# Performance work log

Hardware: AMD Instinct MI355X
Metric: run time of the kernel (lower is better)

Reference implementation:

```python
import jax, jax.numpy as jnp
import numpy as np

N_NODES = 100000
FEAT = 64
HID = 128
N_EDGES = 1200000


def setup_inputs() -> dict:
    key = jax.random.key(0)
    ks = jax.random.split(key, 8)
    x = jax.random.normal(ks[0], (N_NODES, FEAT), dtype=jnp.float32)
    edge_index = jax.random.randint(ks[1], (2, N_EDGES), 0, N_NODES, dtype=jnp.int32)
    # SAGEConv params: lin_l (on aggregated neighbors, with bias), lin_r (on root, no bias)
    W1l = jax.random.normal(ks[2], (HID, FEAT), jnp.float32) / np.float32(np.sqrt(FEAT))
    b1l = jnp.zeros((HID,), jnp.float32)
    W1r = jax.random.normal(ks[3], (HID, FEAT), jnp.float32) / np.float32(np.sqrt(FEAT))
    W2l = jax.random.normal(ks[4], (FEAT, HID), jnp.float32) / np.float32(np.sqrt(HID))
    b2l = jnp.zeros((FEAT,), jnp.float32)
    W2r = jax.random.normal(ks[5], (FEAT, HID), jnp.float32) / np.float32(np.sqrt(HID))
    return {"x": x, "edge_index": edge_index, "W1l": W1l, "b1l": b1l,
            "W1r": W1r, "W2l": W2l, "b2l": b2l, "W2r": W2r}


def _sage_conv(x, src, dst, Wl, bl, Wr, n_nodes):
    # mean aggregation of neighbor messages x[src] at targets dst
    msg = x[src]                                                  # [E, d]
    agg = jax.ops.segment_sum(msg, dst, num_segments=n_nodes)     # [N, d]
    deg = jax.ops.segment_sum(jnp.ones((src.shape[0],), x.dtype), dst,
                              num_segments=n_nodes)               # [N]
    agg = agg / jnp.maximum(deg, 1.0)[:, None]
    # out = lin_l(agg) + lin_r(x); lin_r has no bias (PyG SAGEConv default)
    return agg @ Wl.T + bl + x @ Wr.T


def reference(x, edge_index, W1l, b1l, W1r, W2l, b2l, W2r):
    src, dst = edge_index[0], edge_index[1]
    n = x.shape[0]
    h = jax.nn.relu(_sage_conv(x, src, dst, W1l, b1l, W1r, n))
    # dropout(p=0.5) is identity in eval mode
    out = _sage_conv(h, src, dst, W2l, b2l, W2r, n)
    return out
```

## Files before the change

### kernel.cpp

```cpp
#include <hip/hip_runtime.h>
#include <hip/hip_bf16.h>

typedef __bf16 bf16;
typedef __attribute__((ext_vector_type(8))) __bf16 bf16x8;
typedef __attribute__((ext_vector_type(4))) float f32x4;

#define NBLK 256

__device__ inline void unpack8(uint4 r, f32x4& a, f32x4& b) {
  a.x = __uint_as_float(r.x << 16);
  a.y = __uint_as_float(r.x & 0xffff0000u);
  a.z = __uint_as_float(r.y << 16);
  a.w = __uint_as_float(r.y & 0xffff0000u);
  b.x = __uint_as_float(r.z << 16);
  b.y = __uint_as_float(r.z & 0xffff0000u);
  b.z = __uint_as_float(r.w << 16);
  b.w = __uint_as_float(r.w & 0xffff0000u);
}

__device__ inline uint4 slot_load(const bf16* __restrict__ tab, const int* __restrict__ nbr,
                                  int base, int e, int q, int fo) {
  int idx = base + q;
  uint4 r = make_uint4(0u, 0u, 0u, 0u);
  if (idx < e) {
    int j = nbr[idx];
    r = *(const uint4*)(tab + j * 64 + fo);
  }
  return r;
}

__global__ __launch_bounds__(256) void setup_k(const float* __restrict__ x,
                                               const int* __restrict__ dst,
                                               const float* __restrict__ W1l,
                                               const float* __restrict__ W1r,
                                               const float* __restrict__ W2l,
                                               const float* __restrict__ W2r,
                                               bf16* __restrict__ xb,
                                               bf16* __restrict__ B1,
                                               bf16* __restrict__ B2,
                                               int* __restrict__ hist,
                                               int E, int nb, int N, int Np) {
  __shared__ int h[1024];
  int t = threadIdx.x;
  if (blockIdx.x < NBLK) {
    for (int i = t; i < nb; i += 256) h[i] = 0;
    __syncthreads();
    int chunk = (E + NBLK - 1) / NBLK;
    int s = blockIdx.x * chunk, e = min(E, s + chunk);
    for (int i = s + t; i < e; i += 256) atomicAdd(&h[dst[i] >> 7], 1);
    __syncthreads();
    for (int i = t; i < nb; i += 256) hist[(long)i * NBLK + blockIdx.x] = h[i];
  } else if (blockIdx.x < NBLK + 128) {
    int gid = (blockIdx.x - NBLK) * 256 + t;
    if (gid < 16384) {
      int c = gid >> 7, k = gid & 127;
      float v = (k < 64) ? W1l[c * 64 + k] : W1r[c * 64 + (k - 64)];
      B1[gid] = (bf16)v;
    } else {
      int idx = gid - 16384;
      int n = idx >> 7, k = idx & 127;
      float v = (n < 64) ? W2l[n * 128 + k] : W2r[(n - 64) * 128 + k];
      B2[idx] = (bf16)v;
    }
  } else {
    int gid = (blockIdx.x - NBLK - 128) * 256 + t;
    long base = (long)gid * 4;
    if (base >= (long)Np * 64) return;
    if (base < (long)N * 64) {
      f32x4 v = *(const f32x4*)(x + base);
      bf16 o[4] = {(bf16)v.x, (bf16)v.y, (bf16)v.z, (bf16)v.w};
      *(ulong1*)(xb + base) = *(ulong1*)o;
    } else {
      bf16 o[4] = {(bf16)0.0f, (bf16)0.0f, (bf16)0.0f, (bf16)0.0f};
      *(ulong1*)(xb + base) = *(ulong1*)o;
    }
  }
}

__global__ __launch_bounds__(256) void scanA_k(int* __restrict__ hist,
                                               int* __restrict__ bsum) {
  __shared__ int sd[256];
  int t = threadIdx.x;
  int idx = blockIdx.x * 256 + t;
  int v = hist[idx];
  sd[t] = v;
  __syncthreads();
#pragma unroll
  for (int off = 1; off < 256; off <<= 1) {
    int tv = (t >= off) ? sd[t - off] : 0;
    __syncthreads();
    if (t >= off) sd[t] += tv;
    __syncthreads();
  }
  hist[idx] = sd[t] - v;
  if (t == 255) bsum[blockIdx.x] = sd[255];
}

__global__ __launch_bounds__(1024) void scanB_k(int* __restrict__ bsum, int nb) {
  __shared__ int sd[1024];
  int t = threadIdx.x;
  int v = (t < nb) ? bsum[t] : 0;
  sd[t] = v;
  __syncthreads();
#pragma unroll
  for (int off = 1; off < 1024; off <<= 1) {
    int tv = (t >= off) ? sd[t - off] : 0;
    __syncthreads();
    if (t >= off) sd[t] += tv;
    __syncthreads();
  }
  if (t < nb) bsum[t] = sd[t] - v;
}

__global__ __launch_bounds__(512) void scat_k(const int* __restrict__ src,
                                              const int* __restrict__ dst,
                                              const int* __restrict__ hist,
                                              const int* __restrict__ bsum,
                                              unsigned* __restrict__ ebuf, int E, int nb) {
  __shared__ int cur[1024];
  for (int i = threadIdx.x; i < nb; i += 512)
    cur[i] = bsum[i] + hist[(long)i * NBLK + blockIdx.x];
  __syncthreads();
  int chunk = (E + NBLK - 1) / NBLK;
  int s = blockIdx.x * chunk, e = min(E, s + chunk);
  for (int i = s + threadIdx.x; i < e; i += 512) {
    int d = dst[i];
    int pos = atomicAdd(&cur[d >> 7], 1);
    ebuf[pos] = ((unsigned)src[i] << 7) | (unsigned)(d & 127);
  }
}

__global__ __launch_bounds__(256) void csr_k(const unsigned* __restrict__ ebuf,
                                             const int* __restrict__ bsum,
                                             int* __restrict__ rowptr,
                                             int* __restrict__ nbr, int nb, int Np, int E) {
  __shared__ int hcnt[128];
  __shared__ int hoff[128];
  int b = blockIdx.x, t = threadIdx.x;
  int s = bsum[b];
  int e = (b + 1 < nb) ? bsum[b + 1] : E;
  if (t < 128) hcnt[t] = 0;
  __syncthreads();
  for (int i = s + t; i < e; i += 256) atomicAdd(&hcnt[ebuf[i] & 127u], 1);
  __syncthreads();
  if (t < 128) hoff[t] = hcnt[t];
  __syncthreads();
#pragma unroll
  for (int off = 1; off < 128; off <<= 1) {
    int v = (t < 128 && t >= off) ? hoff[t - off] : 0;
    __syncthreads();
    if (t < 128 && t >= off) hoff[t] += v;
    __syncthreads();
  }
  if (t < 128) {
    int ex = hoff[t] - hcnt[t];
    rowptr[b * 128 + t] = s + ex;
    hcnt[t] = ex;
  }
  if (blockIdx.x == gridDim.x - 1 && t == 0) rowptr[Np] = E;
  __syncthreads();
  for (int i = s + t; i < e; i += 256) {
    unsigned r = ebuf[i];
    int pos = atomicAdd(&hcnt[r & 127u], 1);
    nbr[s + pos] = (int)(r >> 7);
  }
}

__global__ __launch_bounds__(256) void agg1_k(const bf16* __restrict__ xb,
                                              const int* __restrict__ rowptr,
                                              const int* __restrict__ nbr,
                                              bf16* __restrict__ A1, int Np) {
  int wave = threadIdx.x >> 6, lane = threadIdx.x & 63;
  int n0 = (blockIdx.x * 4 + wave) * 4;
  if (n0 >= Np) return;
  int q = lane >> 3, f = lane & 7;
  int fo = f * 8;
  int s[4], e[4];
#pragma unroll
  for (int m = 0; m < 4; m++) { s[m] = rowptr[n0 + m]; e[m] = rowptr[n0 + m + 1]; }
  uint4 c0[4], c1[4];
#pragma unroll
  for (int m = 0; m < 2; m++) {
    c0[m] = slot_load(xb, nbr, s[m], e[m], q, fo);
    c1[m] = slot_load(xb, nbr, s[m] + 8, e[m], q, fo);
  }
  uint4 rvc = (q == 1) ? *(const uint4*)(xb + (long)n0 * 64 + fo)
                       : make_uint4(0u, 0u, 0u, 0u);
#pragma unroll
  for (int m = 0; m < 4; m++) {
    if (m + 2 < 4) {
      c0[m + 2] = slot_load(xb, nbr, s[m + 2], e[m + 2], q, fo);
      c1[m + 2] = slot_load(xb, nbr, s[m + 2] + 8, e[m + 2], q, fo);
    }
    uint4 rvn = (q == 1 && m + 1 < 4)
                    ? *(const uint4*)(xb + (long)(n0 + m + 1) * 64 + fo)
                    : make_uint4(0u, 0u, 0u, 0u);
    f32x4 sa = {0, 0, 0, 0}, sb = {0, 0, 0, 0};
    uint4 a0 = c0[m], a1 = c1[m];
    if (s[m] + 16 < e[m]) {
      for (int i = s[m] + 16; i < e[m]; i += 16) {
        uint4 t0 = slot_load(xb, nbr, i, e[m], q, fo);
        uint4 t1 = slot_load(xb, nbr, i + 8, e[m], q, fo);
        f32x4 a, b;
        unpack8(a0, a, b); sa += a; sb += b;
        unpack8(a1, a, b); sa += a; sb += b;
        a0 = t0; a1 = t1;
      }
    }
    {
      f32x4 a, b;
      unpack8(a0, a, b); sa += a; sb += b;
      unpack8(a1, a, b); sa += a; sb += b;
    }
    float v[8] = {sa.x, sa.y, sa.z, sa.w, sb.x, sb.y, sb.z, sb.w};
#pragma unroll
    for (int k = 0; k < 8; k++) {
      v[k] += __shfl_xor(v[k], 8);
      v[k] += __shfl_xor(v[k], 16);
      v[k] += __shfl_xor(v[k], 32);
    }
    float invd = 1.0f / fmaxf((float)(e[m] - s[m]), 1.0f);
    if (q == 0) {
      bf16x8 o = {(bf16)(v[0] * invd), (bf16)(v[1] * invd), (bf16)(v[2] * invd),
                  (bf16)(v[3] * invd), (bf16)(v[4] * invd), (bf16)(v[5] * invd),
                  (bf16)(v[6] * invd), (bf16)(v[7] * invd)};
      *(bf16x8*)(A1 + (long)(n0 + m) * 128 + fo) = o;
    } else if (q == 1) {
      *(uint4*)(A1 + (long)(n0 + m) * 128 + 64 + fo) = rvc;
    }
    rvc = rvn;
  }
}

__device__ inline int swzoff(int r, int x) {
  return r * 256 + (x ^ (((r & 3) << 6) ^ ((r & 7) << 4)));
}

__global__ __launch_bounds__(256) void fused_k(const bf16* __restrict__ A,
                                               const bf16* __restrict__ B1g,
                                               const bf16* __restrict__ B2g,
                                               const float* __restrict__ b1l,
                                               bf16* __restrict__ Ct,
                                               bf16* __restrict__ Cu, int T) {
  __shared__ __align__(16) char Asm[2][8192];
  __shared__ __align__(16) char Hsm[8192];
  int tid = threadIdx.x;
  int wave = tid >> 6, lane = tid & 63;
  int row = lane & 15, quad = lane >> 4;
  int cb = wave * 32;

  bf16x8 b1f[2][4], b2f[2][4];
#pragma unroll
  for (int jj = 0; jj < 2; jj++)
#pragma unroll
    for (int s = 0; s < 4; s++) {
      b1f[jj][s] = *(const bf16x8*)(B1g + (cb + jj * 16 + row) * 128 + s * 32 + quad * 8);
      b2f[jj][s] = *(const bf16x8*)(B2g + (cb + jj * 16 + row) * 128 + s * 32 + quad * 8);
    }
  float bias[2] = {b1l[cb + row], b1l[cb + 16 + row]};

  int srow = wave * 8 + quad;
  int schunk = row;

  int t = blockIdx.x;
  {
    uint4 v0 = *(const uint4*)(A + ((long)t * 32 + srow) * 128 + schunk * 8);
    uint4 v1 = *(const uint4*)(A + ((long)t * 32 + srow + 4) * 128 + schunk * 8);
    *(uint4*)(Asm[0] + swzoff(srow, schunk * 16)) = v0;
    *(uint4*)(Asm[0] + swzoff(srow + 4, schunk * 16)) = v1;
  }
  __syncthreads();

  int p = 0;
  for (; t < T; t += (int)gridDim.x, p ^= 1) {
    int tn = t + (int)gridDim.x;
    bool pf = tn < T;
    uint4 v0 = {}, v1 = {};
    if (pf) {
      v0 = *(const uint4*)(A + ((long)tn * 32 + srow) * 128 + schunk * 8);
      v1 = *(const uint4*)(A + ((long)tn * 32 + srow + 4) * 128 + schunk * 8);
    }
    f32x4 acc1[2][2] = {};
#pragma unroll
    for (int s = 0; s < 4; s++) {
#pragma unroll
      for (int st = 0; st < 2; st++) {
        bf16x8 a = *(const bf16x8*)(Asm[p] + swzoff(st * 16 + row, s * 64 + quad * 16));
#pragma unroll
        for (int jj = 0; jj < 2; jj++)
          acc1[st][jj] = __builtin_amdgcn_mfma_f32_16x16x32_bf16(a, b1f[jj][s], acc1[st][jj], 0, 0, 0);
      }
    }
#pragma unroll
    for (int st = 0; st < 2; st++)
#pragma unroll
      for (int jj = 0; jj < 2; jj++)
#pragma unroll
        for (int i = 0; i < 4; i++) {
          float v = acc1[st][jj][i] + bias[jj];
          v = v > 0.0f ? v : 0.0f;
          *(bf16*)(Hsm + swzoff(st * 16 + quad * 4 + i, (cb + jj * 16 + row) * 2)) = (bf16)v;
        }
    __syncthreads();
    f32x4 acc2[2][2] = {};
#pragma unroll
    for (int s = 0; s < 4; s++) {
#pragma unroll
      for (int st = 0; st < 2; st++) {
        bf16x8 a = *(const bf16x8*)(Hsm + swzoff(st * 16 + row, s * 64 + quad * 16));
#pragma unroll
        for (int jj = 0; jj < 2; jj++)
          acc2[st][jj] = __builtin_amdgcn_mfma_f32_16x16x32_bf16(a, b2f[jj][s], acc2[st][jj], 0, 0, 0);
      }
    }
    bf16* outp = (wave < 2) ? Ct : Cu;
    int oc = cb + row - ((wave < 2) ? 0 : 64);
#pragma unroll
    for (int st = 0; st < 2; st++)
#pragma unroll
      for (int jj = 0; jj < 2; jj++)
#pragma unroll
        for (int i = 0; i < 4; i++) {
          long grow = (long)t * 32 + st * 16 + quad * 4 + i;
          outp[grow * 64 + oc + jj * 16] = (bf16)acc2[st][jj][i];
        }
    if (pf) {
      *(uint4*)(Asm[p ^ 1] + swzoff(srow, schunk * 16)) = v0;
      *(uint4*)(Asm[p ^ 1] + swzoff(srow + 4, schunk * 16)) = v1;
    }
    __syncthreads();
  }
}

__global__ __launch_bounds__(256) void agg2_k(const bf16* __restrict__ tmat,
                                              const bf16* __restrict__ umat,
                                              const int* __restrict__ rowptr,
                                              const int* __restrict__ nbr,
                                              const float* __restrict__ b2l,
                                              float* __restrict__ out, int N) {
  int wave = threadIdx.x >> 6, lane = threadIdx.x & 63;
  int n = blockIdx.x * 4 + wave;
  if (n >= N) return;
  int s = rowptr[n], e = rowptr[n + 1];
  int q = lane >> 3, f = lane & 7;
  int fo = f * 8;
  f32x4 sa = {0, 0, 0, 0}, sb = {0, 0, 0, 0};
  uint4 c0 = slot_load(tmat, nbr, s, e, q, fo);
  uint4 c1 = slot_load(tmat, nbr, s + 8, e, q, fo);
  int i = s + 16;
  for (; i < e; i += 16) {
    uint4 n0 = slot_load(tmat, nbr, i, e, q, fo);
    uint4 n1 = slot_load(tmat, nbr, i + 8, e, q, fo);
    f32x4 a, b;
    unpack8(c0, a, b); sa += a; sb += b;
    unpack8(c1, a, b); sa += a; sb += b;
    c0 = n0; c1 = n1;
  }
  {
    f32x4 a, b;
    unpack8(c0, a, b); sa += a; sb += b;
    unpack8(c1, a, b); sa += a; sb += b;
  }
  float v[8] = {sa.x, sa.y, sa.z, sa.w, sb.x, sb.y, sb.z, sb.w};
#pragma unroll
  for (int k = 0; k < 8; k++) {
    v[k] += __shfl_xor(v[k], 8);
    v[k] += __shfl_xor(v[k], 16);
    v[k] += __shfl_xor(v[k], 32);
  }
  if (q == 0) {
    float invd = 1.0f / fmaxf((float)(e - s), 1.0f);
    f32x4 b0 = *(const f32x4*)(b2l + fo);
    f32x4 b1 = *(const f32x4*)(b2l + fo + 4);
    f32x4 ua, ub;
    unpack8(*(const uint4*)(umat + n * 64 + fo), ua, ub);
    f32x4 o0, o1;
    o0.x = v[0] * invd + b0.x + ua.x;
    o0.y = v[1] * invd + b0.y + ua.y;
    o0.z = v[2] * invd + b0.z + ua.z;
    o0.w = v[3] * invd + b0.w + ua.w;
    o1.x = v[4] * invd + b1.x + ub.x;
    o1.y = v[5] * invd + b1.y + ub.y;
    o1.z = v[6] * invd + b1.z + ub.z;
    o1.w = v[7] * invd + b1.w + ub.w;
    *(f32x4*)(out + n * 64 + fo) = o0;
    *(f32x4*)(out + n * 64 + fo + 4) = o1;
  }
}

static inline size_t align256(size_t x) { return (x + 255) / 256 * 256; }

extern "C" void kernel_launch(void* const* d_in, const int* in_sizes, int n_in,
                              void* d_out, int out_size, void* d_ws, size_t ws_size,
                              hipStream_t stream) {
  const float* x = (const float*)d_in[0];
  const int* edge_index = (const int*)d_in[1];
  const float* W1l = (const float*)d_in[2];
  const float* b1l = (const float*)d_in[3];
  const float* W1r = (const float*)d_in[4];
  const float* W2l = (const float*)d_in[5];
  const float* b2l = (const float*)d_in[6];
  const float* W2r = (const float*)d_in[7];

  const int N = in_sizes[0] / 64;
  const int E = in_sizes[1] / 2;
  const int Np = (N + 127) / 128 * 128;
  const int nb = Np / 128;
  const int M = nb * NBLK;

  const int* src = edge_index;
  const int* dst = edge_index + E;

  char* ws = (char*)d_ws;
  size_t off = 0;
  int* hist = (int*)(ws + off);           off += align256((size_t)M * 4);
  int* bsum = (int*)(ws + off);           off += align256((size_t)nb * 4);
  int* rowptr = (int*)(ws + off);         off += align256((size_t)(Np + 1) * 4);
  unsigned* ebuf = (unsigned*)(ws + off); off += align256((size_t)E * 4);
  int* nbr = (int*)(ws + off);            off += align256((size_t)E * 4);
  bf16* xb = (bf16*)(ws + off);           off += align256((size_t)Np * 64 * 2);
  bf16* A1 = (bf16*)(ws + off);           off += align256((size_t)Np * 128 * 2);
  bf16* tmat = (bf16*)(ws + off);         off += align256((size_t)Np * 64 * 2);
  bf16* umat = (bf16*)(ws + off);         off += align256((size_t)Np * 64 * 2);
  bf16* B1 = (bf16*)(ws + off);           off += align256(128 * 128 * 2);
  bf16* B2 = (bf16*)(ws + off);           off += align256(128 * 128 * 2);
  float* out = (float*)d_out;

  const int cvtBlocks = (int)(((long)Np * 64 / 4 + 255) / 256);
  setup_k<<<NBLK + 128 + cvtBlocks, 256, 0, stream>>>(x, dst, W1l, W1r, W2l, W2r,
                                                      xb, B1, B2, hist, E, nb, N, Np);
  scanA_k<<<nb, 256, 0, stream>>>(hist, bsum);
  scanB_k<<<1, 1024, 0, stream>>>(bsum, nb);
  scat_k<<<NBLK, 512, 0, stream>>>(src, dst, hist, bsum, ebuf, E, nb);
  csr_k<<<nb, 256, 0, stream>>>(ebuf, bsum, rowptr, nbr, nb, Np, E);

  agg1_k<<<Np / 16, 256, 0, stream>>>(xb, rowptr, nbr, A1, Np);
  fused_k<<<1564, 256, 0, stream>>>(A1, B1, B2, b1l, tmat, umat, Np / 32);
  agg2_k<<<(N + 3) / 4, 256, 0, stream>>>(tmat, umat, rowptr, nbr, b2l, out, N);
}
```

Measured before the change: 220.2 us.

## Build CSR with per-node global atomic counting and scatter instead of two-level bucket sort

```diff
diff --git a/kernel.cpp b/kernel.cpp
--- a/kernel.cpp
+++ b/kernel.cpp
@@ -4,8 +4,6 @@
 typedef __bf16 bf16;
 typedef __attribute__((ext_vector_type(8))) __bf16 bf16x8;
 typedef __attribute__((ext_vector_type(4))) float f32x4;
-
-#define NBLK 256
 
 __device__ inline void unpack8(uint4 r, f32x4& a, f32x4& b) {
   a.x = __uint_as_float(r.x << 16);
@@ -29,29 +27,21 @@
   return r;
 }
 
-__global__ __launch_bounds__(256) void setup_k(const float* __restrict__ x,
-                                               const int* __restrict__ dst,
-                                               const float* __restrict__ W1l,
-                                               const float* __restrict__ W1r,
-                                               const float* __restrict__ W2l,
-                                               const float* __restrict__ W2r,
-                                               bf16* __restrict__ xb,
-                                               bf16* __restrict__ B1,
-                                               bf16* __restrict__ B2,
-                                               int* __restrict__ hist,
-                                               int E, int nb, int N, int Np) {
-  __shared__ int h[1024];
+
+__global__ __launch_bounds__(256) void zero_k(const float* __restrict__ W1l,
+                                              const float* __restrict__ W1r,
+                                              const float* __restrict__ W2l,
+                                              const float* __restrict__ W2r,
+                                              bf16* __restrict__ B1,
+                                              bf16* __restrict__ B2,
+                                              int* __restrict__ deg,
+                                              int Np, int nscan) {
   int t = threadIdx.x;
-  if (blockIdx.x < NBLK) {
-    for (int i = t; i < nb; i += 256) h[i] = 0;
-    __syncthreads();
-    int chunk = (E + NBLK - 1) / NBLK;
-    int s = blockIdx.x * chunk, e = min(E, s + chunk);
-    for (int i = s + t; i < e; i += 256) atomicAdd(&h[dst[i] >> 7], 1);
-    __syncthreads();
-    for (int i = t; i < nb; i += 256) hist[(long)i * NBLK + blockIdx.x] = h[i];
-  } else if (blockIdx.x < NBLK + 128) {
-    int gid = (blockIdx.x - NBLK) * 256 + t;
+  if ((int)blockIdx.x < nscan) {
+    int idx = blockIdx.x * 256 + t;
+    if (idx < Np) deg[idx] = 0;
+  } else {
+    int gid = ((int)blockIdx.x - nscan) * 256 + t;
     if (gid < 16384) {
       int c = gid >> 7, k = gid & 127;
       float v = (k < 64) ? W1l[c * 64 + k] : W1r[c * 64 + (k - 64)];
@@ -62,8 +52,20 @@
       float v = (n < 64) ? W2l[n * 128 + k] : W2r[(n - 64) * 128 + k];
       B2[idx] = (bf16)v;
     }
+  }
+}
+
+__global__ __launch_bounds__(256) void setup_k(const float* __restrict__ x,
+                                               const int* __restrict__ dst,
+                                               int* __restrict__ deg,
+                                               bf16* __restrict__ xb,
+                                               int E, int N, int Np) {
+  int t = threadIdx.x;
+  if (blockIdx.x < 256) {
+    for (int i = blockIdx.x * 256 + t; i < E; i += 256 * 256)
+      atomicAdd(&deg[dst[i]], 1);
   } else {
-    int gid = (blockIdx.x - NBLK - 128) * 256 + t;
+    int gid = (blockIdx.x - 256) * 256 + t;
     long base = (long)gid * 4;
     if (base >= (long)Np * 64) return;
     if (base < (long)N * 64) {
@@ -77,12 +79,13 @@
   }
 }
 
-__global__ __launch_bounds__(256) void scanA_k(int* __restrict__ hist,
-                                               int* __restrict__ bsum) {
+__global__ __launch_bounds__(256) void scan256_k(const int* __restrict__ deg,
+                                                 int* __restrict__ tmp,
+                                                 int* __restrict__ bsum, int Np) {
   __shared__ int sd[256];
   int t = threadIdx.x;
   int idx = blockIdx.x * 256 + t;
-  int v = hist[idx];
+  int v = (idx < Np) ? deg[idx] : 0;
   sd[t] = v;
   __syncthreads();
 #pragma unroll
@@ -92,77 +95,48 @@
     if (t >= off) sd[t] += tv;
     __syncthreads();
   }
-  hist[idx] = sd[t] - v;
+  if (idx < Np) tmp[idx] = sd[t] - v;
   if (t == 255) bsum[blockIdx.x] = sd[255];
 }
 
-__global__ __launch_bounds__(1024) void scanB_k(int* __restrict__ bsum, int nb) {
-  __shared__ int sd[1024];
+__global__ __launch_bounds__(512) void scanS_k(int* __restrict__ bsum, int nv) {
+  __shared__ int sd[512];
   int t = threadIdx.x;
-  int v = (t < nb) ? bsum[t] : 0;
+  int v = (t < nv) ? bsum[t] : 0;
   sd[t] = v;
   __syncthreads();
 #pragma unroll
-  for (int off = 1; off < 1024; off <<= 1) {
+  for (int off = 1; off < 512; off <<= 1) {
     int tv = (t >= off) ? sd[t - off] : 0;
     __syncthreads();
     if (t >= off) sd[t] += tv;
     __syncthreads();
   }
-  if (t < nb) bsum[t] = sd[t] - v;
-}
-
-__global__ __launch_bounds__(512) void scat_k(const int* __restrict__ src,
-                                              const int* __restrict__ dst,
-                                              const int* __restrict__ hist,
-                                              const int* __restrict__ bsum,
-                                              unsigned* __restrict__ ebuf, int E, int nb) {
-  __shared__ int cur[1024];
-  for (int i = threadIdx.x; i < nb; i += 512)
-    cur[i] = bsum[i] + hist[(long)i * NBLK + blockIdx.x];
-  __syncthreads();
-  int chunk = (E + NBLK - 1) / NBLK;
-  int s = blockIdx.x * chunk, e = min(E, s + chunk);
-  for (int i = s + threadIdx.x; i < e; i += 512) {
+  if (t < nv) bsum[t] = sd[t] - v;
+}
+
+__global__ __launch_bounds__(256) void final_k(const int* __restrict__ tmp,
+                                               const int* __restrict__ bsum,
+                                               int* __restrict__ rowptr,
+                                               int* __restrict__ cur, int Np, int E) {
+  int idx = blockIdx.x * 256 + threadIdx.x;
+  if (idx < Np) {
+    int r = tmp[idx] + bsum[idx >> 8];
+    rowptr[idx] = r;
+    cur[idx] = r;
+  } else if (idx == Np) {
+    rowptr[Np] = E;
+  }
+}
+
+__global__ __launch_bounds__(256) void scatter_k(const int* __restrict__ src,
+                                                 const int* __restrict__ dst,
+                                                 int* __restrict__ cur,
+                                                 int* __restrict__ nbr, int E) {
+  for (int i = blockIdx.x * 256 + threadIdx.x; i < E; i += (int)gridDim.x * 256) {
     int d = dst[i];
-    int pos = atomicAdd(&cur[d >> 7], 1);
-    ebuf[pos] = ((unsigned)src[i] << 7) | (unsigned)(d & 127);
-  }
-}
-
-__global__ __launch_bounds__(256) void csr_k(const unsigned* __restrict__ ebuf,
-                                             const int* __restrict__ bsum,
-                                             int* __restrict__ rowptr,
-                                             int* __restrict__ nbr, int nb, int Np, int E) {
-  __shared__ int hcnt[128];
-  __shared__ int hoff[128];
-  int b = blockIdx.x, t = threadIdx.x;
-  int s = bsum[b];
-  int e = (b + 1 < nb) ? bsum[b + 1] : E;
-  if (t < 128) hcnt[t] = 0;
-  __syncthreads();
-  for (int i = s + t; i < e; i += 256) atomicAdd(&hcnt[ebuf[i] & 127u], 1);
-  __syncthreads();
-  if (t < 128) hoff[t] = hcnt[t];
-  __syncthreads();
-#pragma unroll
-  for (int off = 1; off < 128; off <<= 1) {
-    int v = (t < 128 && t >= off) ? hoff[t - off] : 0;
-    __syncthreads();
-    if (t < 128 && t >= off) hoff[t] += v;
-    __syncthreads();
-  }
-  if (t < 128) {
-    int ex = hoff[t] - hcnt[t];
-    rowptr[b * 128 + t] = s + ex;
-    hcnt[t] = ex;
-  }
-  if (blockIdx.x == gridDim.x - 1 && t == 0) rowptr[Np] = E;
-  __syncthreads();
-  for (int i = s + t; i < e; i += 256) {
-    unsigned r = ebuf[i];
-    int pos = atomicAdd(&hcnt[r & 127u], 1);
-    nbr[s + pos] = (int)(r >> 7);
+    int pos = atomicAdd(&cur[d], 1);
+    nbr[pos] = src[i];
   }
 }
 
@@ -405,18 +379,18 @@
   const int N = in_sizes[0] / 64;
   const int E = in_sizes[1] / 2;
   const int Np = (N + 127) / 128 * 128;
-  const int nb = Np / 128;
-  const int M = nb * NBLK;
+  const int nscan = (Np + 255) / 256;
 
   const int* src = edge_index;
   const int* dst = edge_index + E;
 
   char* ws = (char*)d_ws;
   size_t off = 0;
-  int* hist = (int*)(ws + off);           off += align256((size_t)M * 4);
-  int* bsum = (int*)(ws + off);           off += align256((size_t)nb * 4);
+  int* tmp = (int*)(ws + off);            off += align256((size_t)Np * 4);
+  int* bsum = (int*)(ws + off);           off += align256((size_t)nscan * 4);
   int* rowptr = (int*)(ws + off);         off += align256((size_t)(Np + 1) * 4);
-  unsigned* ebuf = (unsigned*)(ws + off); off += align256((size_t)E * 4);
+  int* deg = (int*)(ws + off);            off += align256((size_t)Np * 4);
+  int* cur = (int*)(ws + off);            off += align256((size_t)Np * 4);
   int* nbr = (int*)(ws + off);            off += align256((size_t)E * 4);
   bf16* xb = (bf16*)(ws + off);           off += align256((size_t)Np * 64 * 2);
   bf16* A1 = (bf16*)(ws + off);           off += align256((size_t)Np * 128 * 2);
@@ -427,12 +401,12 @@
   float* out = (float*)d_out;
 
   const int cvtBlocks = (int)(((long)Np * 64 / 4 + 255) / 256);
-  setup_k<<<NBLK + 128 + cvtBlocks, 256, 0, stream>>>(x, dst, W1l, W1r, W2l, W2r,
-                                                      xb, B1, B2, hist, E, nb, N, Np);
-  scanA_k<<<nb, 256, 0, stream>>>(hist, bsum);
-  scanB_k<<<1, 1024, 0, stream>>>(bsum, nb);
-  scat_k<<<NBLK, 512, 0, stream>>>(src, dst, hist, bsum, ebuf, E, nb);
-  csr_k<<<nb, 256, 0, stream>>>(ebuf, bsum, rowptr, nbr, nb, Np, E);
+  zero_k<<<nscan + 128, 256, 0, stream>>>(W1l, W1r, W2l, W2r, B1, B2, deg, Np, nscan);
+  setup_k<<<256 + cvtBlocks, 256, 0, stream>>>(x, dst, deg, xb, E, N, Np);
+  scan256_k<<<nscan, 256, 0, stream>>>(deg, tmp, bsum, Np);
+  scanS_k<<<1, 512, 0, stream>>>(bsum, nscan);
+  final_k<<<nscan + 1, 256, 0, stream>>>(tmp, bsum, rowptr, cur, Np, E);
+  scatter_k<<<1024, 256, 0, stream>>>(src, dst, cur, nbr, E);
 
   agg1_k<<<Np / 16, 256, 0, stream>>>(xb, rowptr, nbr, A1, Np);
   fused_k<<<1564, 256, 0, stream>>>(A1, B1, B2, b1l, tmat, umat, Np / 32);
```

Measured after the change: 330.9 us. 50.3% more time.
